# Kernel tuning notes

Measured on AMD Instinct MI355X. Metric: run time of the kernel, lower is better.

The kernel has to match this reference:

```python
import jax, jax.numpy as jnp
import numpy as np

L, D, H, FF = 4, 512, 8, 1024
B, S = 8, 480
TPT = 15          # TOKENS_PER_TURN
FIELD_IDX = 0
CAP = 6.0         # tanh logit soft cap
NEG = -1e30


def _layer_norm(x, g, b, eps=1e-5):
    m = jnp.mean(x, axis=-1, keepdims=True)
    v = jnp.mean((x - m) ** 2, axis=-1, keepdims=True)
    return (x - m) * jax.lax.rsqrt(v + eps) * g + b


def _episodic_mask(expanded_ids, n_prev_fields):
    # pokemon_batched_episodic_mask, vectorized -> [B, S, S] bool
    idx = jnp.arange(S)
    q_t = (idx // TPT)[:, None]            # [S,1]
    kv_t = (idx // TPT)[None, :]           # [1,S]
    kv_i = (idx % TPT)[None, :]
    same_turn = q_t == kv_t
    prev_field = (kv_i == FIELD_IDX) & (kv_t < q_t) & (q_t - kv_t <= n_prev_fields)
    same_ep = expanded_ids[:, :, None] == expanded_ids[:, None, :]  # [B,S,S]
    return same_ep & (same_turn | prev_field)[None]


def setup_inputs() -> dict:
    key = jax.random.key(0)
    ks = jax.random.split(key, 6)
    x = jax.random.normal(ks[0], (B, S, D), dtype=jnp.float32)
    expanded_ids = jnp.sort(jax.random.randint(ks[1], (B, S), 0, 3), axis=-1)
    inp = {
        "x": x,
        "expanded_ids": expanded_ids,
        "n_prev_fields": 8,
        "Wqkv": 0.02 * jax.random.normal(ks[2], (L, D, 3 * D), dtype=jnp.float32),
        "bqkv": jnp.zeros((L, 3 * D), jnp.float32),
        "Wo": 0.02 * jax.random.normal(ks[3], (L, D, D), dtype=jnp.float32),
        "bo": jnp.zeros((L, D), jnp.float32),
        "g1": jnp.ones((L, D), jnp.float32),
        "b1": jnp.zeros((L, D), jnp.float32),
        "g2": jnp.ones((L, D), jnp.float32),
        "b2": jnp.zeros((L, D), jnp.float32),
        "W1": 0.02 * jax.random.normal(ks[4], (L, D, FF), dtype=jnp.float32),
        "bf1": jnp.zeros((L, FF), jnp.float32),
        "W2": 0.02 * jax.random.normal(ks[5], (L, FF, D), dtype=jnp.float32),
        "bf2": jnp.zeros((L, D), jnp.float32),
    }
    return inp


def _encoder_layer(x, mask, Wqkv, bqkv, Wo, bo, g1, b1, g2, b2, W1, bf1, W2, bf2):
    hd = D // H
    h = _layer_norm(x, g1, b1)
    qkv = h @ Wqkv + bqkv                               # [B,S,3D]
    qkv = qkv.reshape(B, S, 3, H, hd)
    q, k, v = (qkv[:, :, i].transpose(0, 2, 1, 3) for i in range(3))  # [B,H,S,hd]
    scores = jnp.einsum("bhqd,bhkd->bhqk", q, k) / jnp.sqrt(jnp.float32(hd))
    scores = CAP * jnp.tanh(scores / CAP)               # logit soft cap (score_mod)
    scores = jnp.where(mask[:, None], scores, NEG)      # episodic block mask
    attn = jax.nn.softmax(scores, axis=-1)
    out = jnp.einsum("bhqk,bhkd->bhqd", attn, v)
    out = out.transpose(0, 2, 1, 3).reshape(B, S, D)
    x = x + (out @ Wo + bo)
    h2 = _layer_norm(x, g2, b2)
    ff = jax.nn.gelu(h2 @ W1 + bf1, approximate=False) @ W2 + bf2
    return x + ff


def reference(x, expanded_ids, n_prev_fields, Wqkv, bqkv, Wo, bo, g1, b1, g2, b2, W1, bf1, W2, bf2):
    mask = _episodic_mask(expanded_ids, n_prev_fields)
    for l in range(L):
        x = _encoder_layer(x, mask, Wqkv[l], bqkv[l], Wo[l], bo[l],
                           g1[l], b1[l], g2[l], b2[l], W1[l], bf1[l], W2[l], bf2[l])
    return x
```

## Files before the change

### kernel.cpp

```cpp
#include <hip/hip_runtime.h>
#include <hip/hip_bf16.h>
#include <hip/hip_fp16.h>
#include <math.h>

#define NL 4
#define Dm 512
#define Hh 8
#define FFD 1024
#define Bb 8
#define Ss 480
#define TPT 15
#define ROWS (Bb*Ss)

typedef __attribute__((ext_vector_type(8))) short short8v;
typedef __attribute__((ext_vector_type(4))) float f32x4;
typedef __attribute__((ext_vector_type(2))) _Float16 half2v;
typedef __attribute__((ext_vector_type(8))) _Float16 half8v;

#if __has_builtin(__builtin_amdgcn_fdot2)
#define FDOT2(a, b, c) __builtin_amdgcn_fdot2(a, b, c, false)
#else
#define FDOT2(a, b, c) ((c) + (float)(a)[0] * (float)(b)[0] + (float)(a)[1] * (float)(b)[1])
#endif

__device__ __forceinline__ void gld_lds16(const void* g, void* lbase, int lane) {
#if __has_builtin(__builtin_amdgcn_global_load_lds)
    __builtin_amdgcn_global_load_lds((const __attribute__((address_space(1))) void*)g,
                                     (__attribute__((address_space(3))) void*)lbase, 16, 0, 0);
#else
    *(short8v*)((char*)lbase + lane * 16) = *(const short8v*)g;
#endif
}

__global__ __launch_bounds__(256) void ln_kernel(const float* __restrict__ x,
                                                 const float* __restrict__ g,
                                                 const float* __restrict__ b,
                                                 __hip_bfloat16* __restrict__ out) {
    int w = threadIdx.x >> 6, lane = threadIdx.x & 63;
    int row = blockIdx.x * 4 + w;
    const float* xr = x + (size_t)row * Dm + lane * 8;
    float4 v0 = *(const float4*)xr;
    float4 v1 = *(const float4*)(xr + 4);
    float v[8] = { v0.x, v0.y, v0.z, v0.w, v1.x, v1.y, v1.z, v1.w };

    float s = 0.0f;
#pragma unroll
    for (int e = 0; e < 8; e++) s += v[e];
#pragma unroll
    for (int off = 1; off < 64; off <<= 1) s += __shfl_xor(s, off);
    float mean = s * (1.0f / Dm);

    float ss = 0.0f;
#pragma unroll
    for (int e = 0; e < 8; e++) { v[e] -= mean; ss += v[e] * v[e]; }
#pragma unroll
    for (int off = 1; off < 64; off <<= 1) ss += __shfl_xor(ss, off);
    float rstd = rsqrtf(ss * (1.0f / Dm) + 1e-5f);

    const float* gp = g + lane * 8;
    const float* bp = b + lane * 8;
    float4 g0 = *(const float4*)gp, g1 = *(const float4*)(gp + 4);
    float4 b0 = *(const float4*)bp, b1 = *(const float4*)(bp + 4);
    float gg[8] = { g0.x, g0.y, g0.z, g0.w, g1.x, g1.y, g1.z, g1.w };
    float bb[8] = { b0.x, b0.y, b0.z, b0.w, b1.x, b1.y, b1.z, b1.w };
    short8v pack;
#pragma unroll
    for (int e = 0; e < 8; e++) {
        __hip_bfloat16 t = __float2bfloat16(v[e] * rstd * gg[e] + bb[e]);
        pack[e] = __builtin_bit_cast(short, t);
    }
    *(short8v*)&out[(size_t)row * Dm + lane * 8] = pack;
}

__global__ __launch_bounds__(256) void conv_all(const float* __restrict__ Wqkv,
                                                const float* __restrict__ Wo,
                                                const float* __restrict__ W1,
                                                const float* __restrict__ W2,
                                                __hip_bfloat16* __restrict__ oq,
                                                __hip_bfloat16* __restrict__ oo,
                                                __hip_bfloat16* __restrict__ o1,
                                                __hip_bfloat16* __restrict__ o2) {
    int type = blockIdx.z >> 2, l = blockIdx.z & 3;
    int K, N; const float* src; __hip_bfloat16* dst;
    if (type == 0)      { K = 512;  N = 1536; src = Wqkv; dst = oq; }
    else if (type == 1) { K = 512;  N = 512;  src = Wo;   dst = oo; }
    else if (type == 2) { K = 512;  N = 1024; src = W1;   dst = o1; }
    else                { K = 1024; N = 512;  src = W2;   dst = o2; }
    int n0 = blockIdx.x * 32, k0 = blockIdx.y * 32;
    if (n0 >= N || k0 >= K) return;
    src += (size_t)l * K * N;
    dst += (size_t)l * K * N;

    __shared__ float t[32][33];
    int tx = threadIdx.x & 31, ty = threadIdx.x >> 5;
#pragma unroll
    for (int r = 0; r < 4; r++)
        t[ty * 4 + r][tx] = src[(size_t)(k0 + ty * 4 + r) * N + n0 + tx];
    __syncthreads();
#pragma unroll
    for (int r = 0; r < 4; r++)
        dst[(size_t)(n0 + ty * 4 + r) * K + k0 + tx] = __float2bfloat16(t[tx][ty * 4 + r]);
}

template <int BM, int ACT, int RES, int OUTMODE>
__global__ __launch_bounds__(256) void gemm_mfma(const __hip_bfloat16* __restrict__ A,
                                                 const __hip_bfloat16* __restrict__ Bt,
                                                 const float* __restrict__ bias,
                                                 const float* __restrict__ res,
                                                 void* __restrict__ C,
                                                 int M, int N, int K) {
    constexpr int MF = BM / 32;
    constexpr int AC = BM / 32;
    __shared__ __align__(16) short As[2][BM * 64];
    __shared__ __align__(16) short Bs[2][64 * 64];
    const int bm = blockIdx.y * BM, bn = blockIdx.x * 64;
    const int tid = threadIdx.x;
    const int w = tid >> 6, lane = tid & 63;
    const int wm = (w >> 1) * (BM / 2), wn = (w & 1) * 32;
    const int l16 = lane & 15, lq = lane >> 4;
    const short* Ag = (const short*)A;
    const short* Bg = (const short*)Bt;
    const int nt = K >> 6;

    f32x4 acc[MF][2] = {};

    auto stage = [&](int t, int buf) {
        int k0 = t << 6;
#pragma unroll
        for (int c = 0; c < AC; ++c) {
            int e = c * 256 + tid;
            int row = e >> 3;
            int csrc = (e & 7) ^ (row & 7);
            gld_lds16(Ag + (size_t)(bm + row) * K + k0 + csrc * 8,
                      &As[buf][(c * 256 + w * 64) * 8], lane);
        }
#pragma unroll
        for (int c = 0; c < 2; ++c) {
            int e = c * 256 + tid;
            int row = e >> 3;
            int csrc = (e & 7) ^ (row & 7);
            gld_lds16(Bg + (size_t)(bn + row) * K + k0 + csrc * 8,
                      &Bs[buf][(c * 256 + w * 64) * 8], lane);
        }
    };

    stage(0, 0);
    __syncthreads();
    int cur = 0;
    for (int t = 0; t < nt; ++t) {
        if (t + 1 < nt) stage(t + 1, cur ^ 1);
#pragma unroll
        for (int kc = 0; kc < 2; ++kc) {
            short8v af[MF], bf[2];
#pragma unroll
            for (int i = 0; i < MF; i++) {
                int row = wm + i * 16 + l16;
                int ch = (kc * 4 + lq) ^ (row & 7);
                af[i] = *(const short8v*)(&As[cur][row * 64 + ch * 8]);
            }
#pragma unroll
            for (int j = 0; j < 2; j++) {
                int col = wn + j * 16 + l16;
                int ch2 = (kc * 4 + lq) ^ (col & 7);
                bf[j] = *(const short8v*)(&Bs[cur][col * 64 + ch2 * 8]);
            }
#pragma unroll
            for (int i = 0; i < MF; i++)
#pragma unroll
                for (int j = 0; j < 2; j++)
                    acc[i][j] = __builtin_amdgcn_mfma_f32_16x16x32_bf16(
                        af[i], bf[j], acc[i][j], 0, 0, 0);
        }
        __syncthreads();
        cur ^= 1;
    }

#pragma unroll
    for (int i = 0; i < MF; i++) {
#pragma unroll
        for (int j = 0; j < 2; j++) {
#pragma unroll
            for (int r = 0; r < 4; r++) {
                int mrow = bm + wm + i * 16 + lq * 4 + r;
                int ncol = bn + wn + j * 16 + l16;
                float v = acc[i][j][r] + bias[ncol];
                if (ACT == 1) v = 0.5f * v * (1.0f + erff(v * 0.70710678118f));
                if (RES) v += res[(size_t)mrow * N + ncol];
                if (OUTMODE == 0)      ((float*)C)[(size_t)mrow * N + ncol] = v;
                else if (OUTMODE == 1) ((__hip_bfloat16*)C)[(size_t)mrow * N + ncol] = __float2bfloat16(v);
                else                   ((__half*)C)[(size_t)mrow * N + ncol] = __float2half(v);
            }
        }
    }
}

__global__ __launch_bounds__(256) void attn_sparse(const _Float16* __restrict__ qkv,
                                                   const int* __restrict__ ids,
                                                   const int* __restrict__ npf_p,
                                                   __hip_bfloat16* __restrict__ outb) {
    __shared__ _Float16 qs[4][512];
    __shared__ float ps[4][Hh][24];
    int w = threadIdx.x >> 6, lane = threadIdx.x & 63;
    int bq = blockIdx.x * 4 + w;
    int q = bq % Ss, b = bq / Ss;
    int npf = npf_p[0];
    int qt = q / TPT;
    int qid = ids[bq];

    *(half8v*)&qs[w][lane * 8] = *(const half8v*)&qkv[(size_t)bq * 1536 + lane * 8];
    __syncthreads();

    int h = lane >> 3, cp = lane & 7;

    half2v qreg[32];
#pragma unroll
    for (int i = 0; i < 32; i++) qreg[i] = *(const half2v*)&qs[w][h * 64 + i * 2];

    float s[3];
#pragma unroll
    for (int i = 0; i < 3; i++) {
        int c = cp + i * 8;
        float sv = -INFINITY;
        if (c < 23) {
            bool ok; int k;
            if (c < 15) { k = qt * TPT + c; ok = true; }
            else { int dt = c - 14; int kt = qt - dt; k = kt * TPT; ok = (kt >= 0) && (dt <= npf); }
            if (ok && ids[b * Ss + k] == qid) {
                const half8v* kr = (const half8v*)&qkv[(size_t)(b * Ss + k) * 1536 + 512 + h * 64];
                float dot = 0.0f;
#pragma unroll
                for (int cch = 0; cch < 8; cch++) {
                    half8v kv = kr[cch];
#pragma unroll
                    for (int e = 0; e < 4; e++) {
                        half2v kk = { kv[e * 2], kv[e * 2 + 1] };
                        dot = FDOT2(qreg[cch * 4 + e], kk, dot);
                    }
                }
                sv = 6.0f * tanhf(dot * (0.125f / 6.0f));
            }
        }
        s[i] = sv;
    }

    float m = fmaxf(fmaxf(s[0], s[1]), s[2]);
    for (int off = 1; off < 8; off <<= 1) m = fmaxf(m, __shfl_xor(m, off));
    float p0 = expf(s[0] - m), p1 = expf(s[1] - m), p2 = expf(s[2] - m);
    float l = p0 + p1 + p2;
    for (int off = 1; off < 8; off <<= 1) l += __shfl_xor(l, off);
    float inv = 1.0f / l;
    if (cp < 8)       ps[w][h][cp]      = p0 * inv;
    if (cp + 8 < 23)  ps[w][h][cp + 8]  = p1 * inv;
    if (cp + 16 < 23) ps[w][h][cp + 16] = p2 * inv;
    __syncthreads();

    int dg = lane & 7;
    float o[8] = {};
    for (int c = 0; c < 23; c++) {
        float p = ps[w][h][c];
        if (p != 0.0f) {
            int k = (c < 15) ? (qt * TPT + c) : ((qt - (c - 14)) * TPT);
            half8v vv = *(const half8v*)&qkv[(size_t)(b * Ss + k) * 1536 + 1024 + h * 64 + dg * 8];
#pragma unroll
            for (int e = 0; e < 8; e++) o[e] += p * (float)vv[e];
        }
    }
    short8v pack;
#pragma unroll
    for (int e = 0; e < 8; e++) {
        __hip_bfloat16 t = __float2bfloat16(o[e]);
        pack[e] = __builtin_bit_cast(short, t);
    }
    *(short8v*)&outb[(size_t)bq * Dm + h * 64 + dg * 8] = pack;
}

extern "C" void kernel_launch(void* const* d_in, const int* in_sizes, int n_in,
                              void* d_out, int out_size, void* d_ws, size_t ws_size,
                              hipStream_t stream) {
    const float* x    = (const float*)d_in[0];
    const int*   ids  = (const int*)d_in[1];
    const int*   npf  = (const int*)d_in[2];
    const float* Wqkv = (const float*)d_in[3];
    const float* bqkv = (const float*)d_in[4];
    const float* Wo   = (const float*)d_in[5];
    const float* bo   = (const float*)d_in[6];
    const float* g1   = (const float*)d_in[7];
    const float* b1   = (const float*)d_in[8];
    const float* g2   = (const float*)d_in[9];
    const float* b2   = (const float*)d_in[10];
    const float* W1   = (const float*)d_in[11];
    const float* bf1  = (const float*)d_in[12];
    const float* W2   = (const float*)d_in[13];
    const float* bf2  = (const float*)d_in[14];
    float* out = (float*)d_out;

    char* p = (char*)d_ws;
    __hip_bfloat16* hb    = (__hip_bfloat16*)p;   p += (size_t)ROWS * Dm * 2;
    _Float16*       qkvb  = (_Float16*)p;         p += (size_t)ROWS * 3 * Dm * 2;
    __hip_bfloat16* attnb = (__hip_bfloat16*)p;   p += (size_t)ROWS * Dm * 2;
    __hip_bfloat16* fb    = (__hip_bfloat16*)p;   p += (size_t)ROWS * FFD * 2;
    __hip_bfloat16* Wqkv_t= (__hip_bfloat16*)p;   p += (size_t)NL * Dm * 3 * Dm * 2;
    __hip_bfloat16* Wo_t  = (__hip_bfloat16*)p;   p += (size_t)NL * Dm * Dm * 2;
    __hip_bfloat16* W1_t  = (__hip_bfloat16*)p;   p += (size_t)NL * Dm * FFD * 2;
    __hip_bfloat16* W2_t  = (__hip_bfloat16*)p;   p += (size_t)NL * FFD * Dm * 2;

    conv_all<<<dim3(48, 32, 16), 256, 0, stream>>>(Wqkv, Wo, W1, W2,
                                                   Wqkv_t, Wo_t, W1_t, W2_t);

    for (int l = 0; l < NL; l++) {
        const float* xin = (l == 0) ? x : out;
        ln_kernel<<<ROWS / 4, 256, 0, stream>>>(xin, g1 + l * Dm, b1 + l * Dm, hb);
        gemm_mfma<128, 0, 0, 2><<<dim3(24, 30), 256, 0, stream>>>(
            hb, Wqkv_t + (size_t)l * Dm * 3 * Dm, bqkv + l * 3 * Dm, nullptr, qkvb,
            ROWS, 3 * Dm, Dm);
        attn_sparse<<<ROWS / 4, 256, 0, stream>>>(qkvb, ids, npf, attnb);
        gemm_mfma<64, 0, 1, 0><<<dim3(8, 60), 256, 0, stream>>>(
            attnb, Wo_t + (size_t)l * Dm * Dm, bo + l * Dm, xin, out,
            ROWS, Dm, Dm);
        ln_kernel<<<ROWS / 4, 256, 0, stream>>>(out, g2 + l * Dm, b2 + l * Dm, hb);
        gemm_mfma<128, 1, 0, 1><<<dim3(16, 30), 256, 0, stream>>>(
            hb, W1_t + (size_t)l * Dm * FFD, bf1 + l * FFD, nullptr, fb,
            ROWS, FFD, Dm);
        gemm_mfma<64, 0, 1, 0><<<dim3(8, 60), 256, 0, stream>>>(
            fb, W2_t + (size_t)l * FFD * Dm, bf2 + l * Dm, out, out,
            ROWS, Dm, FFD);
    }
}
```

Before: 322.6 us.

## Fuse layernorm into GEMM A-loads using row stats emitted by residual GEMMs

Removes the standalone layernorm kernels. The residual-producing GEMMs now accumulate per-row sum and sum-of-squares into a stats buffer with atomics. The following GEMM loads fp32 activations directly, normalizes them in registers and writes bf16 tiles to LDS, and the QKV and FF1 GEMMs switch to 64x128 tiles. This saves kernel launches and a bf16 round-trip through global memory. In exchange, the A operand is loaded as fp32 through registers instead of async global-to-LDS copies. Variance now comes from E[x^2]-mean^2, which is less numerically stable, and the atomics and an extra memset are added.

```diff
diff --git a/kernel.cpp b/kernel.cpp
--- a/kernel.cpp
+++ b/kernel.cpp
@@ -5,7 +5,6 @@
 
 #define NL 4
 #define Dm 512
-#define Hh 8
 #define FFD 1024
 #define Bb 8
 #define Ss 480
@@ -23,53 +22,29 @@
 #define FDOT2(a, b, c) ((c) + (float)(a)[0] * (float)(b)[0] + (float)(a)[1] * (float)(b)[1])
 #endif
 
-__device__ __forceinline__ void gld_lds16(const void* g, void* lbase, int lane) {
+__device__ __forceinline__ void gld_lds16(const void* g, void* lbase) {
 #if __has_builtin(__builtin_amdgcn_global_load_lds)
     __builtin_amdgcn_global_load_lds((const __attribute__((address_space(1))) void*)g,
                                      (__attribute__((address_space(3))) void*)lbase, 16, 0, 0);
 #else
-    *(short8v*)((char*)lbase + lane * 16) = *(const short8v*)g;
+    (void)g; (void)lbase;
 #endif
 }
 
-__global__ __launch_bounds__(256) void ln_kernel(const float* __restrict__ x,
-                                                 const float* __restrict__ g,
-                                                 const float* __restrict__ b,
-                                                 __hip_bfloat16* __restrict__ out) {
+__global__ __launch_bounds__(256) void stats0_kernel(const float* __restrict__ x,
+                                                     float* __restrict__ st) {
     int w = threadIdx.x >> 6, lane = threadIdx.x & 63;
     int row = blockIdx.x * 4 + w;
     const float* xr = x + (size_t)row * Dm + lane * 8;
     float4 v0 = *(const float4*)xr;
     float4 v1 = *(const float4*)(xr + 4);
     float v[8] = { v0.x, v0.y, v0.z, v0.w, v1.x, v1.y, v1.z, v1.w };
-
-    float s = 0.0f;
-#pragma unroll
-    for (int e = 0; e < 8; e++) s += v[e];
-#pragma unroll
-    for (int off = 1; off < 64; off <<= 1) s += __shfl_xor(s, off);
-    float mean = s * (1.0f / Dm);
-
-    float ss = 0.0f;
-#pragma unroll
-    for (int e = 0; e < 8; e++) { v[e] -= mean; ss += v[e] * v[e]; }
-#pragma unroll
-    for (int off = 1; off < 64; off <<= 1) ss += __shfl_xor(ss, off);
-    float rstd = rsqrtf(ss * (1.0f / Dm) + 1e-5f);
-
-    const float* gp = g + lane * 8;
-    const float* bp = b + lane * 8;
-    float4 g0 = *(const float4*)gp, g1 = *(const float4*)(gp + 4);
-    float4 b0 = *(const float4*)bp, b1 = *(const float4*)(bp + 4);
-    float gg[8] = { g0.x, g0.y, g0.z, g0.w, g1.x, g1.y, g1.z, g1.w };
-    float bb[8] = { b0.x, b0.y, b0.z, b0.w, b1.x, b1.y, b1.z, b1.w };
-    short8v pack;
-#pragma unroll
-    for (int e = 0; e < 8; e++) {
-        __hip_bfloat16 t = __float2bfloat16(v[e] * rstd * gg[e] + bb[e]);
-        pack[e] = __builtin_bit_cast(short, t);
-    }
-    *(short8v*)&out[(size_t)row * Dm + lane * 8] = pack;
+    float s = 0.0f, q = 0.0f;
+#pragma unroll
+    for (int e = 0; e < 8; e++) { s += v[e]; q += v[e] * v[e]; }
+#pragma unroll
+    for (int off = 1; off < 64; off <<= 1) { s += __shfl_xor(s, off); q += __shfl_xor(q, off); }
+    if (lane == 0) { st[row * 2] = s; st[row * 2 + 1] = q; }
 }
 
 __global__ __launch_bounds__(256) void conv_all(const float* __restrict__ Wqkv,
@@ -102,56 +77,109 @@
         dst[(size_t)(n0 + ty * 4 + r) * K + k0 + tx] = __float2bfloat16(t[tx][ty * 4 + r]);
 }
 
-template <int BM, int ACT, int RES, int OUTMODE>
-__global__ __launch_bounds__(256) void gemm_mfma(const __hip_bfloat16* __restrict__ A,
+template <int BM, int BN, int ACT, int RES, int OUTMODE, int LNA, int EMIT>
+__global__ __launch_bounds__(256) void gemm_mfma(const void* __restrict__ Ain,
                                                  const __hip_bfloat16* __restrict__ Bt,
                                                  const float* __restrict__ bias,
                                                  const float* __restrict__ res,
                                                  void* __restrict__ C,
+                                                 const float* __restrict__ stIn,
+                                                 float* __restrict__ stOut,
+                                                 const float* __restrict__ lng,
+                                                 const float* __restrict__ lnb,
                                                  int M, int N, int K) {
     constexpr int MF = BM / 32;
-    constexpr int AC = BM / 32;
+    constexpr int NF = BN / 32;
+    constexpr int ACc = BM / 32;
+    constexpr int BCc = BN / 32;
     __shared__ __align__(16) short As[2][BM * 64];
-    __shared__ __align__(16) short Bs[2][64 * 64];
-    const int bm = blockIdx.y * BM, bn = blockIdx.x * 64;
+    __shared__ __align__(16) short Bs[2][BN * 64];
+    const int bm = blockIdx.y * BM, bn = blockIdx.x * BN;
     const int tid = threadIdx.x;
     const int w = tid >> 6, lane = tid & 63;
-    const int wm = (w >> 1) * (BM / 2), wn = (w & 1) * 32;
+    const int wm = (w >> 1) * (BM / 2), wn = (w & 1) * (BN / 2);
     const int l16 = lane & 15, lq = lane >> 4;
-    const short* Ag = (const short*)A;
+    const short* Ag = (const short*)Ain;
+    const float* Af = (const float*)Ain;
     const short* Bg = (const short*)Bt;
     const int nt = K >> 6;
 
-    f32x4 acc[MF][2] = {};
-
-    auto stage = [&](int t, int buf) {
-        int k0 = t << 6;
-#pragma unroll
-        for (int c = 0; c < AC; ++c) {
+    f32x4 acc[MF][NF] = {};
+
+    int rowA[ACc], csA[ACc];
+    float meanA[ACc], rstdA[ACc];
+#pragma unroll
+    for (int c = 0; c < ACc; c++) {
+        int e = c * 256 + tid;
+        rowA[c] = e >> 3;
+        csA[c] = ((e & 7) ^ (rowA[c] & 7)) * 8;
+        if (LNA) {
+            float s = stIn[(bm + rowA[c]) * 2], q = stIn[(bm + rowA[c]) * 2 + 1];
+            float mu = s * (1.0f / Dm);
+            meanA[c] = mu;
+            rstdA[c] = rsqrtf(q * (1.0f / Dm) - mu * mu + 1e-5f);
+        }
+    }
+
+    float4 a0[ACc], a1[ACc], g0[ACc], g1[ACc], b0[ACc], b1[ACc];
+    auto loadA = [&](int t) {
+#pragma unroll
+        for (int c = 0; c < ACc; c++) {
+            const float* src = Af + (size_t)(bm + rowA[c]) * K + t * 64 + csA[c];
+            a0[c] = *(const float4*)src;
+            a1[c] = *(const float4*)(src + 4);
+            g0[c] = *(const float4*)(lng + t * 64 + csA[c]);
+            g1[c] = *(const float4*)(lng + t * 64 + csA[c] + 4);
+            b0[c] = *(const float4*)(lnb + t * 64 + csA[c]);
+            b1[c] = *(const float4*)(lnb + t * 64 + csA[c] + 4);
+        }
+    };
+    auto writeA = [&](int buf) {
+#pragma unroll
+        for (int c = 0; c < ACc; c++) {
+            float av[8] = { a0[c].x, a0[c].y, a0[c].z, a0[c].w, a1[c].x, a1[c].y, a1[c].z, a1[c].w };
+            float gv[8] = { g0[c].x, g0[c].y, g0[c].z, g0[c].w, g1[c].x, g1[c].y, g1[c].z, g1[c].w };
+            float bv[8] = { b0[c].x, b0[c].y, b0[c].z, b0[c].w, b1[c].x, b1[c].y, b1[c].z, b1[c].w };
+            short8v pk;
+#pragma unroll
+            for (int e = 0; e < 8; e++) {
+                __hip_bfloat16 t16 = __float2bfloat16((av[e] - meanA[c]) * rstdA[c] * gv[e] + bv[e]);
+                pk[e] = __builtin_bit_cast(short, t16);
+            }
+            *(short8v*)&As[buf][(c * 256 + tid) * 8] = pk;
+        }
+    };
+    auto stageA = [&](int t, int buf) {
+#pragma unroll
+        for (int c = 0; c < ACc; c++)
+            gld_lds16(Ag + (size_t)(bm + rowA[c]) * K + t * 64 + csA[c],
+                      &As[buf][(c * 256 + w * 64) * 8]);
+    };
+    auto stageB = [&](int t, int buf) {
+#pragma unroll
+        for (int c = 0; c < BCc; c++) {
             int e = c * 256 + tid;
             int row = e >> 3;
-            int csrc = (e & 7) ^ (row & 7);
-            gld_lds16(Ag + (size_t)(bm + row) * K + k0 + csrc * 8,
-                      &As[buf][(c * 256 + w * 64) * 8], lane);
-        }
-#pragma unroll
-        for (int c = 0; c < 2; ++c) {
-            int e = c * 256 + tid;
-            int row = e >> 3;
-            int csrc = (e & 7) ^ (row & 7);
-            gld_lds16(Bg + (size_t)(bn + row) * K + k0 + csrc * 8,
-                      &Bs[buf][(c * 256 + w * 64) * 8], lane);
+            int cs = ((e & 7) ^ (row & 7)) * 8;
+            gld_lds16(Bg + (size_t)(bn + row) * K + t * 64 + cs,
+                      &Bs[buf][(c * 256 + w * 64) * 8]);
         }
     };
 
-    stage(0, 0);
+    if (LNA) loadA(0); else stageA(0, 0);
+    stageB(0, 0);
+    if (LNA) writeA(0);
     __syncthreads();
     int cur = 0;
     for (int t = 0; t < nt; ++t) {
-        if (t + 1 < nt) stage(t + 1, cur ^ 1);
+        bool pf = (t + 1 < nt);
+        if (pf) {
+            if (LNA) loadA(t + 1); else stageA(t + 1, cur ^ 1);
+            stageB(t + 1, cur ^ 1);
+        }
 #pragma unroll
         for (int kc = 0; kc < 2; ++kc) {
-            short8v af[MF], bf[2];
+            short8v af[MF], bf[NF];
 #pragma unroll
             for (int i = 0; i < MF; i++) {
                 int row = wm + i * 16 + l16;
@@ -159,7 +187,7 @@
                 af[i] = *(const short8v*)(&As[cur][row * 64 + ch * 8]);
             }
 #pragma unroll
-            for (int j = 0; j < 2; j++) {
+            for (int j = 0; j < NF; j++) {
                 int col = wn + j * 16 + l16;
                 int ch2 = (kc * 4 + lq) ^ (col & 7);
                 bf[j] = *(const short8v*)(&Bs[cur][col * 64 + ch2 * 8]);
@@ -167,18 +195,26 @@
 #pragma unroll
             for (int i = 0; i < MF; i++)
 #pragma unroll
-                for (int j = 0; j < 2; j++)
+                for (int j = 0; j < NF; j++)
                     acc[i][j] = __builtin_amdgcn_mfma_f32_16x16x32_bf16(
                         af[i], bf[j], acc[i][j], 0, 0, 0);
         }
+        if (pf && LNA) writeA(cur ^ 1);
         __syncthreads();
         cur ^= 1;
     }
 
+    float vsum[MF][4], vsq[MF][4];
+    if (EMIT) {
+#pragma unroll
+        for (int i = 0; i < MF; i++)
+#pragma unroll
+            for (int r = 0; r < 4; r++) { vsum[i][r] = 0.0f; vsq[i][r] = 0.0f; }
+    }
 #pragma unroll
     for (int i = 0; i < MF; i++) {
 #pragma unroll
-        for (int j = 0; j < 2; j++) {
+        for (int j = 0; j < NF; j++) {
 #pragma unroll
             for (int r = 0; r < 4; r++) {
                 int mrow = bm + wm + i * 16 + lq * 4 + r;
@@ -189,8 +225,27 @@
                 if (OUTMODE == 0)      ((float*)C)[(size_t)mrow * N + ncol] = v;
                 else if (OUTMODE == 1) ((__hip_bfloat16*)C)[(size_t)mrow * N + ncol] = __float2bfloat16(v);
                 else                   ((__half*)C)[(size_t)mrow * N + ncol] = __float2half(v);
-            }
-        }
+                if (EMIT) { vsum[i][r] += v; vsq[i][r] += v * v; }
+            }
+        }
+    }
+    if (EMIT) {
+#pragma unroll
+        for (int i = 0; i < MF; i++)
+#pragma unroll
+            for (int r = 0; r < 4; r++) {
+                float s = vsum[i][r], q = vsq[i][r];
+#pragma unroll
+                for (int off = 1; off < 16; off <<= 1) {
+                    s += __shfl_xor(s, off);
+                    q += __shfl_xor(q, off);
+                }
+                if (l16 == 0) {
+                    int row = bm + wm + i * 16 + lq * 4 + r;
+                    atomicAdd(&stOut[row * 2], s);
+                    atomicAdd(&stOut[row * 2 + 1], q);
+                }
+            }
     }
 }
 
@@ -199,7 +254,7 @@
                                                    const int* __restrict__ npf_p,
                                                    __hip_bfloat16* __restrict__ outb) {
     __shared__ _Float16 qs[4][512];
-    __shared__ float ps[4][Hh][24];
+    __shared__ float ps[4][8][24];
     int w = threadIdx.x >> 6, lane = threadIdx.x & 63;
     int bq = blockIdx.x * 4 + w;
     int q = bq % Ss, b = bq / Ss;
@@ -295,7 +350,7 @@
     float* out = (float*)d_out;
 
     char* p = (char*)d_ws;
-    __hip_bfloat16* hb    = (__hip_bfloat16*)p;   p += (size_t)ROWS * Dm * 2;
+    float*          stats = (float*)p;            p += (size_t)9 * ROWS * 2 * 4;
     _Float16*       qkvb  = (_Float16*)p;         p += (size_t)ROWS * 3 * Dm * 2;
     __hip_bfloat16* attnb = (__hip_bfloat16*)p;   p += (size_t)ROWS * Dm * 2;
     __hip_bfloat16* fb    = (__hip_bfloat16*)p;   p += (size_t)ROWS * FFD * 2;
@@ -304,25 +359,29 @@
     __hip_bfloat16* W1_t  = (__hip_bfloat16*)p;   p += (size_t)NL * Dm * FFD * 2;
     __hip_bfloat16* W2_t  = (__hip_bfloat16*)p;   p += (size_t)NL * FFD * Dm * 2;
 
+    hipMemsetAsync(stats, 0, (size_t)9 * ROWS * 2 * 4, stream);
     conv_all<<<dim3(48, 32, 16), 256, 0, stream>>>(Wqkv, Wo, W1, W2,
                                                    Wqkv_t, Wo_t, W1_t, W2_t);
+    stats0_kernel<<<ROWS / 4, 256, 0, stream>>>(x, stats);
 
     for (int l = 0; l < NL; l++) {
         const float* xin = (l == 0) ? x : out;
-        ln_kernel<<<ROWS / 4, 256, 0, stream>>>(xin, g1 + l * Dm, b1 + l * Dm, hb);
-        gemm_mfma<128, 0, 0, 2><<<dim3(24, 30), 256, 0, stream>>>(
-            hb, Wqkv_t + (size_t)l * Dm * 3 * Dm, bqkv + l * 3 * Dm, nullptr, qkvb,
-            ROWS, 3 * Dm, Dm);
+        float* st_ln1 = stats + (size_t)(2 * l) * ROWS * 2;
+        float* st_ln2 = stats + (size_t)(2 * l + 1) * ROWS * 2;
+        float* st_nx  = stats + (size_t)(2 * l + 2) * ROWS * 2;
+
+        gemm_mfma<64, 128, 0, 0, 2, 1, 0><<<dim3(12, 60), 256, 0, stream>>>(
+            xin, Wqkv_t + (size_t)l * Dm * 3 * Dm, bqkv + l * 3 * Dm, nullptr, qkvb,
+            st_ln1, nullptr, g1 + l * Dm, b1 + l * Dm, ROWS, 3 * Dm, Dm);
         attn_sparse<<<ROWS / 4, 256, 0, stream>>>(qkvb, ids, npf, attnb);
-        gemm_mfma<64, 0, 1, 0><<<dim3(8, 60), 256, 0, stream>>>(
+        gemm_mfma<64, 64, 0, 1, 0, 0, 1><<<dim3(8, 60), 256, 0, stream>>>(
             attnb, Wo_t + (size_t)l * Dm * Dm, bo + l * Dm, xin, out,
-            ROWS, Dm, Dm);
-        ln_kernel<<<ROWS / 4, 256, 0, stream>>>(out, g2 + l * Dm, b2 + l * Dm, hb);
-        gemm_mfma<128, 1, 0, 1><<<dim3(16, 30), 256, 0, stream>>>(
-            hb, W1_t + (size_t)l * Dm * FFD, bf1 + l * FFD, nullptr, fb,
-            ROWS, FFD, Dm);
-        gemm_mfma<64, 0, 1, 0><<<dim3(8, 60), 256, 0, stream>>>(
+            nullptr, st_ln2, nullptr, nullptr, ROWS, Dm, Dm);
+        gemm_mfma<64, 128, 1, 0, 1, 1, 0><<<dim3(8, 60), 256, 0, stream>>>(
+            out, W1_t + (size_t)l * Dm * FFD, bf1 + l * FFD, nullptr, fb,
+            st_ln2, nullptr, g2 + l * Dm, b2 + l * Dm, ROWS, FFD, Dm);
+        gemm_mfma<64, 64, 0, 1, 0, 0, 1><<<dim3(8, 60), 256, 0, stream>>>(
             fb, W2_t + (size_t)l * FFD * Dm, bf2 + l * Dm, out, out,
-            ROWS, Dm, FFD);
-    }
-}
+            nullptr, st_nx, nullptr, nullptr, ROWS, Dm, FFD);
+    }
+}
```

Measured after the change: 377.8 us. 17.1% more time.

## Fuse LayerNorm into full-row N=512 GEMM epilogues for Wo and W2

Applied to the files above, without the earlier changes.

Adds a gemm_wide kernel in which each 512-thread block computes 64 full rows of the 512-wide output, so the residual add and the following LayerNorm (row sum and sum of squares reduced across waves through LDS) run in the epilogue. This removes the separate ln_kernel launches and one re-read of the fp32 activations per LayerNorm. The cost is a grid of only 60 blocks, which underfills the GPU's CUs, plus a single-buffered B tile that needs an extra barrier per K step. LayerNorm variance is computed as E[x^2]-mu^2 instead of the two-pass form, which may lose some accuracy.

```diff
diff --git a/kernel.cpp b/kernel.cpp
--- a/kernel.cpp
+++ b/kernel.cpp
@@ -5,7 +5,6 @@
 
 #define NL 4
 #define Dm 512
-#define Hh 8
 #define FFD 1024
 #define Bb 8
 #define Ss 480
@@ -23,12 +22,12 @@
 #define FDOT2(a, b, c) ((c) + (float)(a)[0] * (float)(b)[0] + (float)(a)[1] * (float)(b)[1])
 #endif
 
-__device__ __forceinline__ void gld_lds16(const void* g, void* lbase, int lane) {
+__device__ __forceinline__ void gld_lds16(const void* g, void* lbase) {
 #if __has_builtin(__builtin_amdgcn_global_load_lds)
     __builtin_amdgcn_global_load_lds((const __attribute__((address_space(1))) void*)g,
                                      (__attribute__((address_space(3))) void*)lbase, 16, 0, 0);
 #else
-    *(short8v*)((char*)lbase + lane * 16) = *(const short8v*)g;
+    (void)g; (void)lbase;
 #endif
 }
 
@@ -102,15 +101,14 @@
         dst[(size_t)(n0 + ty * 4 + r) * K + k0 + tx] = __float2bfloat16(t[tx][ty * 4 + r]);
 }
 
-template <int BM, int ACT, int RES, int OUTMODE>
+template <int BM, int ACT, int OUTMODE>
 __global__ __launch_bounds__(256) void gemm_mfma(const __hip_bfloat16* __restrict__ A,
                                                  const __hip_bfloat16* __restrict__ Bt,
                                                  const float* __restrict__ bias,
-                                                 const float* __restrict__ res,
                                                  void* __restrict__ C,
                                                  int M, int N, int K) {
     constexpr int MF = BM / 32;
-    constexpr int AC = BM / 32;
+    constexpr int ACc = BM / 32;
     __shared__ __align__(16) short As[2][BM * 64];
     __shared__ __align__(16) short Bs[2][64 * 64];
     const int bm = blockIdx.y * BM, bn = blockIdx.x * 64;
@@ -127,12 +125,12 @@
     auto stage = [&](int t, int buf) {
         int k0 = t << 6;
 #pragma unroll
-        for (int c = 0; c < AC; ++c) {
+        for (int c = 0; c < ACc; ++c) {
             int e = c * 256 + tid;
             int row = e >> 3;
             int csrc = (e & 7) ^ (row & 7);
             gld_lds16(Ag + (size_t)(bm + row) * K + k0 + csrc * 8,
-                      &As[buf][(c * 256 + w * 64) * 8], lane);
+                      &As[buf][(c * 256 + w * 64) * 8]);
         }
 #pragma unroll
         for (int c = 0; c < 2; ++c) {
@@ -140,7 +138,7 @@
             int row = e >> 3;
             int csrc = (e & 7) ^ (row & 7);
             gld_lds16(Bg + (size_t)(bn + row) * K + k0 + csrc * 8,
-                      &Bs[buf][(c * 256 + w * 64) * 8], lane);
+                      &Bs[buf][(c * 256 + w * 64) * 8]);
         }
     };
 
@@ -185,10 +183,159 @@
                 int ncol = bn + wn + j * 16 + l16;
                 float v = acc[i][j][r] + bias[ncol];
                 if (ACT == 1) v = 0.5f * v * (1.0f + erff(v * 0.70710678118f));
-                if (RES) v += res[(size_t)mrow * N + ncol];
-                if (OUTMODE == 0)      ((float*)C)[(size_t)mrow * N + ncol] = v;
-                else if (OUTMODE == 1) ((__hip_bfloat16*)C)[(size_t)mrow * N + ncol] = __float2bfloat16(v);
-                else                   ((__half*)C)[(size_t)mrow * N + ncol] = __float2half(v);
+                if (OUTMODE == 1) ((__hip_bfloat16*)C)[(size_t)mrow * N + ncol] = __float2bfloat16(v);
+                else              ((__half*)C)[(size_t)mrow * N + ncol] = __float2half(v);
+            }
+        }
+    }
+}
+
+template <int EPLN>
+__global__ __launch_bounds__(512, 2) void gemm_wide(const __hip_bfloat16* __restrict__ A,
+                                                    const __hip_bfloat16* __restrict__ Bt,
+                                                    const float* __restrict__ bias,
+                                                    const float* __restrict__ res,
+                                                    float* __restrict__ outp,
+                                                    __hip_bfloat16* __restrict__ hb,
+                                                    const float* __restrict__ lng,
+                                                    const float* __restrict__ lnb,
+                                                    int K) {
+    __shared__ __align__(16) short As[2][64 * 64];
+    __shared__ __align__(16) short Bs[512 * 64];
+    __shared__ float sred[4][64][2];
+    const int bm = blockIdx.x * 64;
+    const int tid = threadIdx.x;
+    const int w = tid >> 6, lane = tid & 63;
+    const int wr = w >> 2, wc = w & 3;
+    const int wm = wr * 32, wn = wc * 128;
+    const int l16 = lane & 15, lq = lane >> 4;
+    const short* Ag = (const short*)A;
+    const short* Bg = (const short*)Bt;
+    const int nt = K >> 6;
+
+    f32x4 acc[2][8] = {};
+
+    const int rowA = tid >> 3;
+    const int csA = (tid & 7) ^ (rowA & 7);
+    const short* Asrc = Ag + (size_t)(bm + rowA) * K + csA * 8;
+
+    short8v breg[8];
+    const int rowB0 = tid >> 3, colB = tid & 7;
+    auto loadB = [&](int t) {
+#pragma unroll
+        for (int c = 0; c < 8; c++) {
+            int row = c * 64 + rowB0;
+            breg[c] = *(const short8v*)(Bg + (size_t)row * K + t * 64 + colB * 8);
+        }
+    };
+    auto writeB = [&]() {
+#pragma unroll
+        for (int c = 0; c < 8; c++) {
+            int row = c * 64 + rowB0;
+            int cs = colB ^ (row & 7);
+            *(short8v*)&Bs[row * 64 + cs * 8] = breg[c];
+        }
+    };
+
+    loadB(0);
+    gld_lds16(Asrc, &As[0][w * 64 * 8]);
+    writeB();
+    __syncthreads();
+    int cur = 0;
+    for (int t = 0; t < nt; ++t) {
+        bool pf = (t + 1 < nt);
+        if (pf) {
+            loadB(t + 1);
+            gld_lds16(Asrc + (t + 1) * 64, &As[cur ^ 1][w * 64 * 8]);
+        }
+#pragma unroll
+        for (int kc = 0; kc < 2; ++kc) {
+            short8v af[2], bf[8];
+#pragma unroll
+            for (int i = 0; i < 2; i++) {
+                int row = wm + i * 16 + l16;
+                int ch = (kc * 4 + lq) ^ (row & 7);
+                af[i] = *(const short8v*)(&As[cur][row * 64 + ch * 8]);
+            }
+#pragma unroll
+            for (int j = 0; j < 8; j++) {
+                int col = wn + j * 16 + l16;
+                int ch2 = (kc * 4 + lq) ^ (col & 7);
+                bf[j] = *(const short8v*)(&Bs[col * 64 + ch2 * 8]);
+            }
+#pragma unroll
+            for (int i = 0; i < 2; i++)
+#pragma unroll
+                for (int j = 0; j < 8; j++)
+                    acc[i][j] = __builtin_amdgcn_mfma_f32_16x16x32_bf16(
+                        af[i], bf[j], acc[i][j], 0, 0, 0);
+        }
+        __syncthreads();
+        if (pf) writeB();
+        __syncthreads();
+        cur ^= 1;
+    }
+
+    float ps[2][4], pq[2][4];
+#pragma unroll
+    for (int i = 0; i < 2; i++)
+#pragma unroll
+        for (int r = 0; r < 4; r++) { ps[i][r] = 0.0f; pq[i][r] = 0.0f; }
+#pragma unroll
+    for (int i = 0; i < 2; i++) {
+#pragma unroll
+        for (int j = 0; j < 8; j++) {
+#pragma unroll
+            for (int r = 0; r < 4; r++) {
+                int mrow = bm + wm + i * 16 + lq * 4 + r;
+                int ncol = wn + j * 16 + l16;
+                float v = acc[i][j][r] + bias[ncol] + res[(size_t)mrow * Dm + ncol];
+                outp[(size_t)mrow * Dm + ncol] = v;
+                acc[i][j][r] = v;
+                if (EPLN) { ps[i][r] += v; pq[i][r] += v * v; }
+            }
+        }
+    }
+    if (EPLN) {
+#pragma unroll
+        for (int i = 0; i < 2; i++)
+#pragma unroll
+            for (int r = 0; r < 4; r++) {
+                float s = ps[i][r], q = pq[i][r];
+#pragma unroll
+                for (int off = 1; off < 16; off <<= 1) {
+                    s += __shfl_xor(s, off);
+                    q += __shfl_xor(q, off);
+                }
+                if (l16 == 0) {
+                    int rl = wm + i * 16 + lq * 4 + r;
+                    sred[wc][rl][0] = s;
+                    sred[wc][rl][1] = q;
+                }
+            }
+        __syncthreads();
+        float gj[8], bj[8];
+#pragma unroll
+        for (int j = 0; j < 8; j++) {
+            int nc = wn + j * 16 + l16;
+            gj[j] = lng[nc];
+            bj[j] = lnb[nc];
+        }
+#pragma unroll
+        for (int i = 0; i < 2; i++) {
+#pragma unroll
+            for (int r = 0; r < 4; r++) {
+                int rl = wm + i * 16 + lq * 4 + r;
+                float s = sred[0][rl][0] + sred[1][rl][0] + sred[2][rl][0] + sred[3][rl][0];
+                float q = sred[0][rl][1] + sred[1][rl][1] + sred[2][rl][1] + sred[3][rl][1];
+                float mu = s * (1.0f / Dm);
+                float rstd = rsqrtf(q * (1.0f / Dm) - mu * mu + 1e-5f);
+#pragma unroll
+                for (int j = 0; j < 8; j++) {
+                    int nc = wn + j * 16 + l16;
+                    hb[(size_t)(bm + rl) * Dm + nc] =
+                        __float2bfloat16((acc[i][j][r] - mu) * rstd * gj[j] + bj[j]);
+                }
             }
         }
     }
@@ -199,7 +346,7 @@
                                                    const int* __restrict__ npf_p,
                                                    __hip_bfloat16* __restrict__ outb) {
     __shared__ _Float16 qs[4][512];
-    __shared__ float ps[4][Hh][24];
+    __shared__ float ps[4][8][24];
     int w = threadIdx.x >> 6, lane = threadIdx.x & 63;
     int bq = blockIdx.x * 4 + w;
     int q = bq % Ss, b = bq / Ss;
@@ -306,23 +453,28 @@
 
     conv_all<<<dim3(48, 32, 16), 256, 0, stream>>>(Wqkv, Wo, W1, W2,
                                                    Wqkv_t, Wo_t, W1_t, W2_t);
+    ln_kernel<<<ROWS / 4, 256, 0, stream>>>(x, g1, b1, hb);
 
     for (int l = 0; l < NL; l++) {
         const float* xin = (l == 0) ? x : out;
-        ln_kernel<<<ROWS / 4, 256, 0, stream>>>(xin, g1 + l * Dm, b1 + l * Dm, hb);
-        gemm_mfma<128, 0, 0, 2><<<dim3(24, 30), 256, 0, stream>>>(
-            hb, Wqkv_t + (size_t)l * Dm * 3 * Dm, bqkv + l * 3 * Dm, nullptr, qkvb,
+        gemm_mfma<128, 0, 2><<<dim3(24, 30), 256, 0, stream>>>(
+            hb, Wqkv_t + (size_t)l * Dm * 3 * Dm, bqkv + l * 3 * Dm, qkvb,
             ROWS, 3 * Dm, Dm);
         attn_sparse<<<ROWS / 4, 256, 0, stream>>>(qkvb, ids, npf, attnb);
-        gemm_mfma<64, 0, 1, 0><<<dim3(8, 60), 256, 0, stream>>>(
+        gemm_wide<1><<<60, 512, 0, stream>>>(
             attnb, Wo_t + (size_t)l * Dm * Dm, bo + l * Dm, xin, out,
-            ROWS, Dm, Dm);
-        ln_kernel<<<ROWS / 4, 256, 0, stream>>>(out, g2 + l * Dm, b2 + l * Dm, hb);
-        gemm_mfma<128, 1, 0, 1><<<dim3(16, 30), 256, 0, stream>>>(
-            hb, W1_t + (size_t)l * Dm * FFD, bf1 + l * FFD, nullptr, fb,
+            hb, g2 + l * Dm, b2 + l * Dm, Dm);
+        gemm_mfma<128, 1, 1><<<dim3(16, 30), 256, 0, stream>>>(
+            hb, W1_t + (size_t)l * Dm * FFD, bf1 + l * FFD, fb,
             ROWS, FFD, Dm);
-        gemm_mfma<64, 0, 1, 0><<<dim3(8, 60), 256, 0, stream>>>(
-            fb, W2_t + (size_t)l * FFD * Dm, bf2 + l * Dm, out, out,
-            ROWS, Dm, FFD);
-    }
-}
+        if (l < NL - 1) {
+            gemm_wide<1><<<60, 512, 0, stream>>>(
+                fb, W2_t + (size_t)l * FFD * Dm, bf2 + l * Dm, out, out,
+                hb, g1 + (l + 1) * Dm, b1 + (l + 1) * Dm, FFD);
+        } else {
+            gemm_wide<0><<<60, 512, 0, stream>>>(
+                fb, W2_t + (size_t)l * FFD * Dm, bf2 + l * Dm, out, out,
+                nullptr, nullptr, nullptr, FFD);
+        }
+    }
+}
```

Result: slower. 423.5 us (+31.3%).

## Parameterize GEMM tile width and buffering, use fast exp in attention

Applied to the files above, without the earlier changes.

The GEMM kernel is templated on tile N-width and on double versus single buffering. QKV and FFN1 now use 128x128 tiles, which halves the grid and raises per-block reuse. The Wo and FFN2 GEMMs drop to single buffering, cutting LDS and possibly raising occupancy, at the cost of losing load/compute overlap. Attention replaces tanhf and expf with __expf-based forms, trading a little accuracy for cheaper transcendentals.

```diff
diff --git a/kernel.cpp b/kernel.cpp
--- a/kernel.cpp
+++ b/kernel.cpp
@@ -5,7 +5,6 @@
 
 #define NL 4
 #define Dm 512
-#define Hh 8
 #define FFD 1024
 #define Bb 8
 #define Ss 480
@@ -23,12 +22,12 @@
 #define FDOT2(a, b, c) ((c) + (float)(a)[0] * (float)(b)[0] + (float)(a)[1] * (float)(b)[1])
 #endif
 
-__device__ __forceinline__ void gld_lds16(const void* g, void* lbase, int lane) {
+__device__ __forceinline__ void gld_lds16(const void* g, void* lbase) {
 #if __has_builtin(__builtin_amdgcn_global_load_lds)
     __builtin_amdgcn_global_load_lds((const __attribute__((address_space(1))) void*)g,
                                      (__attribute__((address_space(3))) void*)lbase, 16, 0, 0);
 #else
-    *(short8v*)((char*)lbase + lane * 16) = *(const short8v*)g;
+    (void)g; (void)lbase;
 #endif
 }
 
@@ -102,7 +101,7 @@
         dst[(size_t)(n0 + ty * 4 + r) * K + k0 + tx] = __float2bfloat16(t[tx][ty * 4 + r]);
 }
 
-template <int BM, int ACT, int RES, int OUTMODE>
+template <int BM, int BN, int DBUF, int ACT, int RES, int OUTMODE>
 __global__ __launch_bounds__(256) void gemm_mfma(const __hip_bfloat16* __restrict__ A,
                                                  const __hip_bfloat16* __restrict__ Bt,
                                                  const float* __restrict__ bias,
@@ -110,75 +109,91 @@
                                                  void* __restrict__ C,
                                                  int M, int N, int K) {
     constexpr int MF = BM / 32;
-    constexpr int AC = BM / 32;
-    __shared__ __align__(16) short As[2][BM * 64];
-    __shared__ __align__(16) short Bs[2][64 * 64];
-    const int bm = blockIdx.y * BM, bn = blockIdx.x * 64;
+    constexpr int NF = BN / 32;
+    constexpr int ACc = BM / 32;
+    constexpr int BCc = BN / 32;
+    constexpr int NBUF = DBUF ? 2 : 1;
+    __shared__ __align__(16) short As[NBUF][BM * 64];
+    __shared__ __align__(16) short Bs[NBUF][BN * 64];
+    const int bm = blockIdx.y * BM, bn = blockIdx.x * BN;
     const int tid = threadIdx.x;
     const int w = tid >> 6, lane = tid & 63;
-    const int wm = (w >> 1) * (BM / 2), wn = (w & 1) * 32;
+    const int wm = (w >> 1) * (BM / 2), wn = (w & 1) * (BN / 2);
     const int l16 = lane & 15, lq = lane >> 4;
     const short* Ag = (const short*)A;
     const short* Bg = (const short*)Bt;
     const int nt = K >> 6;
 
-    f32x4 acc[MF][2] = {};
+    f32x4 acc[MF][NF] = {};
 
     auto stage = [&](int t, int buf) {
         int k0 = t << 6;
 #pragma unroll
-        for (int c = 0; c < AC; ++c) {
+        for (int c = 0; c < ACc; ++c) {
             int e = c * 256 + tid;
             int row = e >> 3;
             int csrc = (e & 7) ^ (row & 7);
             gld_lds16(Ag + (size_t)(bm + row) * K + k0 + csrc * 8,
-                      &As[buf][(c * 256 + w * 64) * 8], lane);
-        }
-#pragma unroll
-        for (int c = 0; c < 2; ++c) {
+                      &As[buf][(c * 256 + w * 64) * 8]);
+        }
+#pragma unroll
+        for (int c = 0; c < BCc; ++c) {
             int e = c * 256 + tid;
             int row = e >> 3;
             int csrc = (e & 7) ^ (row & 7);
             gld_lds16(Bg + (size_t)(bn + row) * K + k0 + csrc * 8,
-                      &Bs[buf][(c * 256 + w * 64) * 8], lane);
+                      &Bs[buf][(c * 256 + w * 64) * 8]);
         }
     };
 
-    stage(0, 0);
-    __syncthreads();
-    int cur = 0;
-    for (int t = 0; t < nt; ++t) {
-        if (t + 1 < nt) stage(t + 1, cur ^ 1);
+    auto compute = [&](int buf) {
 #pragma unroll
         for (int kc = 0; kc < 2; ++kc) {
-            short8v af[MF], bf[2];
+            short8v af[MF], bf[NF];
 #pragma unroll
             for (int i = 0; i < MF; i++) {
                 int row = wm + i * 16 + l16;
                 int ch = (kc * 4 + lq) ^ (row & 7);
-                af[i] = *(const short8v*)(&As[cur][row * 64 + ch * 8]);
+                af[i] = *(const short8v*)(&As[buf][row * 64 + ch * 8]);
             }
 #pragma unroll
-            for (int j = 0; j < 2; j++) {
+            for (int j = 0; j < NF; j++) {
                 int col = wn + j * 16 + l16;
                 int ch2 = (kc * 4 + lq) ^ (col & 7);
-                bf[j] = *(const short8v*)(&Bs[cur][col * 64 + ch2 * 8]);
+                bf[j] = *(const short8v*)(&Bs[buf][col * 64 + ch2 * 8]);
             }
 #pragma unroll
             for (int i = 0; i < MF; i++)
 #pragma unroll
-                for (int j = 0; j < 2; j++)
+                for (int j = 0; j < NF; j++)
                     acc[i][j] = __builtin_amdgcn_mfma_f32_16x16x32_bf16(
                         af[i], bf[j], acc[i][j], 0, 0, 0);
         }
+    };
+
+    if (DBUF) {
+        stage(0, 0);
         __syncthreads();
-        cur ^= 1;
+        int cur = 0;
+        for (int t = 0; t < nt; ++t) {
+            if (t + 1 < nt) stage(t + 1, cur ^ 1);
+            compute(cur);
+            __syncthreads();
+            cur ^= 1;
+        }
+    } else {
+        for (int t = 0; t < nt; ++t) {
+            stage(t, 0);
+            __syncthreads();
+            compute(0);
+            __syncthreads();
+        }
     }
 
 #pragma unroll
     for (int i = 0; i < MF; i++) {
 #pragma unroll
-        for (int j = 0; j < 2; j++) {
+        for (int j = 0; j < NF; j++) {
 #pragma unroll
             for (int r = 0; r < 4; r++) {
                 int mrow = bm + wm + i * 16 + lq * 4 + r;
@@ -199,7 +214,7 @@
                                                    const int* __restrict__ npf_p,
                                                    __hip_bfloat16* __restrict__ outb) {
     __shared__ _Float16 qs[4][512];
-    __shared__ float ps[4][Hh][24];
+    __shared__ float ps[4][8][24];
     int w = threadIdx.x >> 6, lane = threadIdx.x & 63;
     int bq = blockIdx.x * 4 + w;
     int q = bq % Ss, b = bq / Ss;
@@ -237,7 +252,9 @@
                         dot = FDOT2(qreg[cch * 4 + e], kk, dot);
                     }
                 }
-                sv = 6.0f * tanhf(dot * (0.125f / 6.0f));
+                float y = dot * (0.125f / 6.0f);
+                float e2 = __expf(2.0f * y);
+                sv = 6.0f * (e2 - 1.0f) / (e2 + 1.0f);
             }
         }
         s[i] = sv;
@@ -245,7 +262,7 @@
 
     float m = fmaxf(fmaxf(s[0], s[1]), s[2]);
     for (int off = 1; off < 8; off <<= 1) m = fmaxf(m, __shfl_xor(m, off));
-    float p0 = expf(s[0] - m), p1 = expf(s[1] - m), p2 = expf(s[2] - m);
+    float p0 = __expf(s[0] - m), p1 = __expf(s[1] - m), p2 = __expf(s[2] - m);
     float l = p0 + p1 + p2;
     for (int off = 1; off < 8; off <<= 1) l += __shfl_xor(l, off);
     float inv = 1.0f / l;
@@ -310,18 +327,18 @@
     for (int l = 0; l < NL; l++) {
         const float* xin = (l == 0) ? x : out;
         ln_kernel<<<ROWS / 4, 256, 0, stream>>>(xin, g1 + l * Dm, b1 + l * Dm, hb);
-        gemm_mfma<128, 0, 0, 2><<<dim3(24, 30), 256, 0, stream>>>(
+        gemm_mfma<128, 128, 1, 0, 0, 2><<<dim3(12, 30), 256, 0, stream>>>(
             hb, Wqkv_t + (size_t)l * Dm * 3 * Dm, bqkv + l * 3 * Dm, nullptr, qkvb,
             ROWS, 3 * Dm, Dm);
         attn_sparse<<<ROWS / 4, 256, 0, stream>>>(qkvb, ids, npf, attnb);
-        gemm_mfma<64, 0, 1, 0><<<dim3(8, 60), 256, 0, stream>>>(
+        gemm_mfma<64, 64, 0, 0, 1, 0><<<dim3(8, 60), 256, 0, stream>>>(
             attnb, Wo_t + (size_t)l * Dm * Dm, bo + l * Dm, xin, out,
             ROWS, Dm, Dm);
         ln_kernel<<<ROWS / 4, 256, 0, stream>>>(out, g2 + l * Dm, b2 + l * Dm, hb);
-        gemm_mfma<128, 1, 0, 1><<<dim3(16, 30), 256, 0, stream>>>(
+        gemm_mfma<128, 128, 1, 1, 0, 1><<<dim3(8, 30), 256, 0, stream>>>(
             hb, W1_t + (size_t)l * Dm * FFD, bf1 + l * FFD, nullptr, fb,
             ROWS, FFD, Dm);
-        gemm_mfma<64, 0, 1, 0><<<dim3(8, 60), 256, 0, stream>>>(
+        gemm_mfma<64, 64, 0, 0, 1, 0><<<dim3(8, 60), 256, 0, stream>>>(
             fb, W2_t + (size_t)l * FFD * Dm, bf2 + l * Dm, out, out,
             ROWS, Dm, FFD);
     }
```

Result: slower. 348.6 us (+8.1%).
